# Optimization experiments

Measured on AMD Instinct MI355X. Metric: run time of the kernel, lower is better.

Reference implementation:

```python
import jax, jax.numpy as jnp
import numpy as np

B, S, D, H = 2, 2048, 1024, 16
DH = D // H
SCALE = 1.0 / float(np.sqrt(DH))


def setup_inputs() -> dict:
    key = jax.random.key(0)
    ks = jax.random.split(key, 5)
    x = jax.random.normal(ks[0], (B, S, D), dtype=jnp.float32)
    init = 0.02
    Wq = jax.random.normal(ks[1], (D, D), dtype=jnp.float32) * init
    Wk = jax.random.normal(ks[2], (D, D), dtype=jnp.float32) * init
    Wv = jax.random.normal(ks[3], (D, D), dtype=jnp.float32) * init
    Wo = jax.random.normal(ks[4], (D, D), dtype=jnp.float32) * init
    bq = jnp.zeros((D,), dtype=jnp.float32)
    bk = jnp.zeros((D,), dtype=jnp.float32)
    bv = jnp.zeros((D,), dtype=jnp.float32)
    bo = jnp.zeros((D,), dtype=jnp.float32)
    return {"x": x, "Wq": Wq, "bq": bq, "Wk": Wk, "bk": bk,
            "Wv": Wv, "bv": bv, "Wo": Wo, "bo": bo}


def reference(x, Wq, bq, Wk, bk, Wv, bv, Wo, bo):
    # torch Linear: y = x @ W.T + b  (W: [out, in])
    q = x @ Wq.T + bq  # [B,S,D]
    k = x @ Wk.T + bk
    v = x @ Wv.T + bv
    # split heads -> [B,H,S,dh]
    q = q.reshape(B, S, H, DH).transpose(0, 2, 1, 3)
    k = k.reshape(B, S, H, DH).transpose(0, 2, 1, 3)
    v = v.reshape(B, S, H, DH).transpose(0, 2, 1, 3)
    scores = jnp.einsum('bhqd,bhkd->bhqk', q, k) * SCALE  # [B,H,S,S]
    p = jax.nn.softmax(scores, axis=-1)
    o = jnp.einsum('bhqk,bhkd->bhqd', p, v)  # [B,H,S,dh]
    # faithful to original: view(B, d_model, S) then transpose(-1,-2)
    o = o.reshape(B, D, S).swapaxes(-1, -2)  # [B,S,D]
    return o @ Wo.T + bo
```

## Files before the change

### kernel.cpp

```cpp
#include <hip/hip_runtime.h>
#include <cstdint>
#include <cstddef>


typedef _Float16 h16;
typedef _Float16 h16x8 __attribute__((ext_vector_type(8)));
typedef _Float16 h16x4 __attribute__((ext_vector_type(4)));
typedef float    f32x4 __attribute__((ext_vector_type(4)));

#define MFMA16 __builtin_amdgcn_mfma_f32_16x16x32_f16

#define QSCALE 0.1803368801111204f

__device__ __forceinline__ void gload_lds16(char* lds_dst, const void* gsrc) {
  __builtin_amdgcn_global_load_lds(
      (__attribute__((address_space(1))) void*)gsrc,
      (__attribute__((address_space(3))) void*)lds_dst,
      16, 0, 0);
}


__global__ __launch_bounds__(256)
void cast_all(const float* __restrict__ x,
              const float* __restrict__ wq, const float* __restrict__ wk,
              const float* __restrict__ wv, const float* __restrict__ wo,
              h16* __restrict__ xb, h16* __restrict__ wqb, h16* __restrict__ wkb,
              h16* __restrict__ wvb, h16* __restrict__ wob) {
  const int z = blockIdx.y;
  const float* src; h16* dst; int n4;
  switch (z) {
    case 0:  src = x;  dst = xb;  n4 = 1048576; break;
    case 1:  src = wq; dst = wqb; n4 = 262144;  break;
    case 2:  src = wk; dst = wkb; n4 = 262144;  break;
    case 3:  src = wv; dst = wvb; n4 = 262144;  break;
    default: src = wo; dst = wob; n4 = 262144;  break;
  }
  int i = blockIdx.x * 256 + threadIdx.x;
  const int stride = gridDim.x * 256;
  for (; i < n4; i += stride) {
    float4 v = reinterpret_cast<const float4*>(src)[i];
    h16x4 o = { (h16)v.x, (h16)v.y, (h16)v.z, (h16)v.w };
    reinterpret_cast<h16x4*>(dst)[i] = o;
  }
}

__device__ __forceinline__ void gemm_core_128(
    const h16* __restrict__ A, const h16* __restrict__ W,
    char* lds, f32x4 (&acc)[4][4])
{
  const int tid  = threadIdx.x;
  const int lane = tid & 63;
  const int w    = tid >> 6;
  const int wr   = w >> 1, wc = w & 1;
  const int blockRow = blockIdx.y * 128;
  const int blockCol = blockIdx.x * 128;

  const int sr  = (tid >> 2) & 15;
  const int sc  = tid & 3;
  const int skc = sc ^ ((sr >> 1) & 3);

  const h16* srcA0 = A + (size_t)(blockRow + (0 * 4 + w) * 16 + sr) * 1024 + skc * 8;
  const h16* srcA1 = A + (size_t)(blockRow + (1 * 4 + w) * 16 + sr) * 1024 + skc * 8;
  const h16* srcB0 = W + (size_t)(blockCol + (0 * 4 + w) * 16 + sr) * 1024 + skc * 8;
  const h16* srcB1 = W + (size_t)(blockCol + (1 * 4 + w) * 16 + sr) * 1024 + skc * 8;

  const int dA0o = w * 1024;
  const int dA1o = 4096 + w * 1024;
  const int dB0o = 8192 + w * 1024;
  const int dB1o = 12288 + w * 1024;

  const int fr = lane & 15, fg = lane >> 4;
  const int foff = fr * 64 + ((fg ^ ((fr >> 1) & 3)) << 4);

#pragma unroll
  for (int i = 0; i < 4; ++i)
#pragma unroll
    for (int j = 0; j < 4; ++j) acc[i][j] = f32x4{0.f, 0.f, 0.f, 0.f};

  gload_lds16(lds + dA0o, srcA0);
  gload_lds16(lds + dA1o, srcA1);
  gload_lds16(lds + dB0o, srcB0);
  gload_lds16(lds + dB1o, srcB1);

  for (int ks = 0; ks < 32; ++ks) {
    char* buf = lds + (ks & 1) * 16384;
    __syncthreads();
    if (ks != 31) {
      char* nbuf = lds + ((ks & 1) ^ 1) * 16384;
      gload_lds16(nbuf + dA0o, srcA0 + (ks + 1) * 32);
      gload_lds16(nbuf + dA1o, srcA1 + (ks + 1) * 32);
      gload_lds16(nbuf + dB0o, srcB0 + (ks + 1) * 32);
      gload_lds16(nbuf + dB1o, srcB1 + (ks + 1) * 32);
    }
    char* ldsA = buf;
    char* ldsB = buf + 8192;

    h16x8 af[4], bfv[4];
#pragma unroll
    for (int t = 0; t < 4; ++t)
      af[t] = *(const h16x8*)(ldsA + (wr * 4 + t) * 1024 + foff);
#pragma unroll
    for (int t = 0; t < 4; ++t)
      bfv[t] = *(const h16x8*)(ldsB + (wc * 4 + t) * 1024 + foff);
#pragma unroll
    for (int i = 0; i < 4; ++i)
#pragma unroll
      for (int j = 0; j < 4; ++j)
        acc[i][j] = MFMA16(af[i], bfv[j], acc[i][j], 0, 0, 0);
  }
}

__global__ __launch_bounds__(256, 2)
void gemm_qkv(const h16* __restrict__ xb,
              const h16* __restrict__ wq, const h16* __restrict__ wk, const h16* __restrict__ wv,
              const float* __restrict__ bq, const float* __restrict__ bk, const float* __restrict__ bv,
              h16* __restrict__ q_, h16* __restrict__ k_, h16* __restrict__ vt_)
{
  __shared__ alignas(128) char lds[32768];
  const int z = blockIdx.z;
  const h16* W = (z == 0) ? wq : (z == 1) ? wk : wv;
  const float* bias = (z == 0) ? bq : (z == 1) ? bk : bv;

  f32x4 acc[4][4];
  gemm_core_128(xb, W, lds, acc);

  const int lane = threadIdx.x & 63;
  const int w = threadIdx.x >> 6;
  const int wr = w >> 1, wc = w & 1;
  const int fr = lane & 15, fg = lane >> 4;
  const int blockRow = blockIdx.y * 128;
  const int blockCol = blockIdx.x * 128;

  if (z == 2) {
#pragma unroll
    for (int ct = 0; ct < 4; ++ct) {
      int n = blockCol + wc * 64 + ct * 16 + fr;
      int hh = n >> 6, dd = n & 63;
      float bv_ = bias[n];
#pragma unroll
      for (int rt = 0; rt < 4; ++rt) {
        int m = blockRow + wr * 64 + rt * 16 + 4 * fg;
        int bb = m >> 11, s0 = m & 2047;
        h16x4 pack = { (h16)(acc[rt][ct][0] + bv_), (h16)(acc[rt][ct][1] + bv_),
                       (h16)(acc[rt][ct][2] + bv_), (h16)(acc[rt][ct][3] + bv_) };
        *(h16x4*)(vt_ + ((size_t)((bb * 16 + hh) * 64 + dd)) * 2048 + s0) = pack;
      }
    }
  } else {
    const float scl = (z == 0) ? QSCALE : 1.0f;
    h16* dst = (z == 0) ? q_ : k_;
#pragma unroll
    for (int ct = 0; ct < 4; ++ct) {
      int n = blockCol + wc * 64 + ct * 16 + fr;
      float bv_ = bias[n];
#pragma unroll
      for (int rt = 0; rt < 4; ++rt) {
        int m0 = blockRow + wr * 64 + rt * 16 + 4 * fg;
#pragma unroll
        for (int r = 0; r < 4; ++r)
          dst[(size_t)(m0 + r) * 1024 + n] = (h16)((acc[rt][ct][r] + bv_) * scl);
      }
    }
  }
}

__global__ __launch_bounds__(256, 2)
void gemm_out(const h16* __restrict__ yt, const h16* __restrict__ wo,
              const float* __restrict__ bo, float* __restrict__ out)
{
  __shared__ alignas(128) char lds[32768];
  f32x4 acc[4][4];
  gemm_core_128(yt, wo, lds, acc);

  const int lane = threadIdx.x & 63;
  const int w = threadIdx.x >> 6;
  const int wr = w >> 1, wc = w & 1;
  const int fr = lane & 15, fg = lane >> 4;
  const int blockRow = blockIdx.y * 128;
  const int blockCol = blockIdx.x * 128;

#pragma unroll
  for (int ct = 0; ct < 4; ++ct) {
    int n = blockCol + wc * 64 + ct * 16 + fr;
    float bv_ = bo[n];
#pragma unroll
    for (int rt = 0; rt < 4; ++rt) {
      int m0 = blockRow + wr * 64 + rt * 16 + 4 * fg;
#pragma unroll
      for (int r = 0; r < 4; ++r)
        out[(size_t)(m0 + r) * 1024 + n] = acc[rt][ct][r] + bv_;
    }
  }
}

__global__ __launch_bounds__(256, 2)
void attn_kernel(const h16* __restrict__ qb, const h16* __restrict__ kb,
                 const h16* __restrict__ vtb, h16* __restrict__ ytb)
{
  __shared__ alignas(128) char lds[32768 + 20480];
  const int tid = threadIdx.x, lane = tid & 63, w = tid >> 6;
  const int fr = lane & 15, fg = lane >> 4;

  const int orig = blockIdx.x;
  const int wgid = (orig & 7) * 64 + (orig >> 3);
  const int p  = wgid & 15;
  const int hh = (wgid >> 4) & 15;
  const int b  = wgid >> 8;

  char* ldsP_A = lds + 32768 + w * 5120;
  char* ldsP_B = ldsP_A + 2560;

  const int aq = w * 16 + fr;
  const h16* qrowA = qb + ((size_t)(b * 2048 + 32 * aq + p)) * 1024 + hh * 64;
  const h16* qrowB = qrowA + 16 * 1024;
  h16x8 qfA0 = *(const h16x8*)(qrowA + fg * 8);
  h16x8 qfA1 = *(const h16x8*)(qrowA + 32 + fg * 8);
  h16x8 qfB0 = *(const h16x8*)(qrowB + fg * 8);
  h16x8 qfB1 = *(const h16x8*)(qrowB + 32 + fg * 8);

  const int sr  = (tid >> 2) & 15;
  const int sc  = tid & 3;
  const int skc = sc ^ ((sr >> 1) & 3);
  const int rloc0 = (w >> 1) * 16 + sr;
  const int rloc1 = ((4 + w) >> 1) * 16 + sr;
  const int kc0 = (w & 1) * 32 + skc * 8;
  const int kc1 = ((4 + w) & 1) * 32 + skc * 8;

  const h16* srcK0 = kb + ((size_t)(b * 2048 + rloc0)) * 1024 + hh * 64 + kc0;
  const h16* srcK1 = kb + ((size_t)(b * 2048 + rloc1)) * 1024 + hh * 64 + kc1;
  const h16* srcV0 = vtb + ((size_t)((b * 16 + hh) * 64 + rloc0)) * 2048 + kc0;
  const h16* srcV1 = vtb + ((size_t)((b * 16 + hh) * 64 + rloc1)) * 2048 + kc1;

  const int dK0o = w * 1024, dK1o = 4096 + w * 1024;
  const int dV0o = 8192 + w * 1024, dV1o = 12288 + w * 1024;

  const int foff = fr * 64 + ((fg ^ ((fr >> 1) & 3)) << 4);

  f32x4 oA[4], oB[4];
#pragma unroll
  for (int i = 0; i < 4; ++i) { oA[i] = f32x4{0.f,0.f,0.f,0.f}; oB[i] = f32x4{0.f,0.f,0.f,0.f}; }
  float lA = 0.f, lB = 0.f;

  gload_lds16(lds + dK0o, srcK0);
  gload_lds16(lds + dK1o, srcK1);
  gload_lds16(lds + dV0o, srcV0);
  gload_lds16(lds + dV1o, srcV1);

  for (int ch = 0; ch < 32; ++ch) {
    char* buf = lds + (ch & 1) * 16384;
    __syncthreads();
    if (ch != 31) {
      char* nbuf = lds + ((ch & 1) ^ 1) * 16384;
      gload_lds16(nbuf + dK0o, srcK0 + (size_t)(ch + 1) * 65536);
      gload_lds16(nbuf + dK1o, srcK1 + (size_t)(ch + 1) * 65536);
      gload_lds16(nbuf + dV0o, srcV0 + (size_t)(ch + 1) * 64);
      gload_lds16(nbuf + dV1o, srcV1 + (size_t)(ch + 1) * 64);
    }
    char* ldsK = buf;
    char* ldsV = buf + 8192;

#pragma unroll
    for (int t = 0; t < 4; ++t) {
      h16x8 kf0 = *(const h16x8*)(ldsK + (t * 2 + 0) * 1024 + foff);
      h16x8 kf1 = *(const h16x8*)(ldsK + (t * 2 + 1) * 1024 + foff);
      f32x4 sA = f32x4{0.f,0.f,0.f,0.f};
      sA = MFMA16(kf0, qfA0, sA, 0, 0, 0);
      sA = MFMA16(kf1, qfA1, sA, 0, 0, 0);
      f32x4 sB = f32x4{0.f,0.f,0.f,0.f};
      sB = MFMA16(kf0, qfB0, sB, 0, 0, 0);
      sB = MFMA16(kf1, qfB1, sB, 0, 0, 0);
      float a0 = exp2f(sA[0]), a1 = exp2f(sA[1]), a2 = exp2f(sA[2]), a3 = exp2f(sA[3]);
      float c0 = exp2f(sB[0]), c1 = exp2f(sB[1]), c2 = exp2f(sB[2]), c3 = exp2f(sB[3]);
      h16x4 pkA = { (h16)a0, (h16)a1, (h16)a2, (h16)a3 };
      h16x4 pkB = { (h16)c0, (h16)c1, (h16)c2, (h16)c3 };
      *(h16x4*)(ldsP_A + fr * 160 + t * 32 + fg * 8) = pkA;
      *(h16x4*)(ldsP_B + fr * 160 + t * 32 + fg * 8) = pkB;
      lA += (a0 + a1) + (a2 + a3);
      lB += (c0 + c1) + (c2 + c3);
    }

    h16x8 pfA0 = *(const h16x8*)(ldsP_A + fr * 160 + fg * 16);
    h16x8 pfA1 = *(const h16x8*)(ldsP_A + fr * 160 + 64 + fg * 16);
    h16x8 pfB0 = *(const h16x8*)(ldsP_B + fr * 160 + fg * 16);
    h16x8 pfB1 = *(const h16x8*)(ldsP_B + fr * 160 + 64 + fg * 16);

#pragma unroll
    for (int dt = 0; dt < 4; ++dt) {
      h16x8 vf0 = *(const h16x8*)(ldsV + (dt * 2 + 0) * 1024 + foff);
      h16x8 vf1 = *(const h16x8*)(ldsV + (dt * 2 + 1) * 1024 + foff);
      oA[dt] = MFMA16(pfA0, vf0, oA[dt], 0, 0, 0);
      oA[dt] = MFMA16(pfA1, vf1, oA[dt], 0, 0, 0);
      oB[dt] = MFMA16(pfB0, vf0, oB[dt], 0, 0, 0);
      oB[dt] = MFMA16(pfB1, vf1, oB[dt], 0, 0, 0);
    }
  }

  lA += __shfl_xor(lA, 16); lA += __shfl_xor(lA, 32);
  lB += __shfl_xor(lB, 16); lB += __shfl_xor(lB, 32);
  float iA = 1.0f / lA, iB = 1.0f / lB;
  float iAr[4], iBr[4];
#pragma unroll
  for (int r = 0; r < 4; ++r) {
    int src = (lane & 48) | (4 * fg + r);
    iAr[r] = __shfl(iA, src);
    iBr[r] = __shfl(iB, src);
  }

#pragma unroll
  for (int dt = 0; dt < 4; ++dt) {
    int row = dt * 16 + fr;
    size_t colb = (size_t)(hh * 64 + w * 16 + fg * 4);
    h16x4 sA4 = { (h16)(oA[dt][0] * iAr[0]), (h16)(oA[dt][1] * iAr[1]),
                  (h16)(oA[dt][2] * iAr[2]), (h16)(oA[dt][3] * iAr[3]) };
    h16x4 sB4 = { (h16)(oB[dt][0] * iBr[0]), (h16)(oB[dt][1] * iBr[1]),
                  (h16)(oB[dt][2] * iBr[2]), (h16)(oB[dt][3] * iBr[3]) };
    *(h16x4*)(ytb + ((size_t)(b * 2048 + p * 64 + row)) * 1024 + colb) = sA4;
    *(h16x4*)(ytb + ((size_t)(b * 2048 + (p + 16) * 64 + row)) * 1024 + colb) = sB4;
  }
}

extern "C" void kernel_launch(void* const* d_in, const int* in_sizes, int n_in,
                              void* d_out, int out_size, void* d_ws, size_t ws_size,
                              hipStream_t stream) {
  const float* x  = (const float*)d_in[0];
  const float* Wq = (const float*)d_in[1];
  const float* bq = (const float*)d_in[2];
  const float* Wk = (const float*)d_in[3];
  const float* bk = (const float*)d_in[4];
  const float* Wv = (const float*)d_in[5];
  const float* bv = (const float*)d_in[6];
  const float* Wo = (const float*)d_in[7];
  const float* bo = (const float*)d_in[8];

  char* ws = (char*)d_ws;
  h16* xb  = (h16*)(ws);
  h16* wqb = (h16*)(ws + (size_t)(8  << 20));
  h16* wkb = (h16*)(ws + (size_t)(10 << 20));
  h16* wvb = (h16*)(ws + (size_t)(12 << 20));
  h16* wob = (h16*)(ws + (size_t)(14 << 20));
  h16* q_  = (h16*)(ws + (size_t)(16 << 20));
  h16* k_  = (h16*)(ws + (size_t)(24 << 20));
  h16* vt_ = (h16*)(ws + (size_t)(32 << 20));
  h16* yt_ = (h16*)(ws + (size_t)(40 << 20));

  cast_all<<<dim3(512, 5), 256, 0, stream>>>(x, Wq, Wk, Wv, Wo, xb, wqb, wkb, wvb, wob);
  gemm_qkv<<<dim3(8, 32, 3), 256, 0, stream>>>(xb, wqb, wkb, wvb, bq, bk, bv, q_, k_, vt_);
  attn_kernel<<<512, 256, 0, stream>>>(q_, k_, vt_, yt_);
  gemm_out<<<dim3(8, 32, 1), 256, 0, stream>>>(yt_, wob, bo, (float*)d_out);
}
```

Baseline: 132.0 us.

## Keep softmax probabilities in registers via permlane swaps instead of LDS round-trip

The attention kernel stops writing the exponentiated scores to LDS and reading them back as MFMA A-operands. Instead it packs them with cvt_pkrtz, permutes K rows so the score layout matches the operand layout, and exchanges halves between lanes with v_permlane32_swap. Row sums now use fdot2 on the packed halves, exp2 uses the hardware builtin, and s_setprio brackets the MFMA sections. This removes LDS traffic and one barrier-free dependency per chunk and shrinks LDS use, which may allow more occupancy, at the cost of relying on an exact lane-permutation mapping.

```diff
diff --git a/kernel.cpp b/kernel.cpp
--- a/kernel.cpp
+++ b/kernel.cpp
@@ -6,17 +6,48 @@
 typedef _Float16 h16;
 typedef _Float16 h16x8 __attribute__((ext_vector_type(8)));
 typedef _Float16 h16x4 __attribute__((ext_vector_type(4)));
+typedef _Float16 h16x2 __attribute__((ext_vector_type(2)));
 typedef float    f32x4 __attribute__((ext_vector_type(4)));
+typedef unsigned int u32x4 __attribute__((ext_vector_type(4)));
 
 #define MFMA16 __builtin_amdgcn_mfma_f32_16x16x32_f16
 
 #define QSCALE 0.1803368801111204f
+
+#if __has_builtin(__builtin_amdgcn_exp2f)
+#define EXP2F(x) __builtin_amdgcn_exp2f(x)
+#else
+#define EXP2F(x) exp2f(x)
+#endif
 
 __device__ __forceinline__ void gload_lds16(char* lds_dst, const void* gsrc) {
   __builtin_amdgcn_global_load_lds(
       (__attribute__((address_space(1))) void*)gsrc,
       (__attribute__((address_space(3))) void*)lds_dst,
       16, 0, 0);
+}
+
+__device__ __forceinline__ unsigned pk2(float lo, float hi) {
+  return __builtin_bit_cast(unsigned, __builtin_amdgcn_cvt_pkrtz(lo, hi));
+}
+
+__device__ __forceinline__ float dot2a(unsigned p, float acc) {
+#if __has_builtin(__builtin_amdgcn_fdot2)
+  const h16x2 one = {(h16)1.f, (h16)1.f};
+  return __builtin_amdgcn_fdot2(__builtin_bit_cast(h16x2, p), one, acc, false);
+#else
+  h16x2 v = __builtin_bit_cast(h16x2, p);
+  return acc + (float)v[0] + (float)v[1];
+#endif
+}
+
+__device__ __forceinline__ void swap32(unsigned& a, unsigned& b) {
+  asm("v_permlane32_swap_b32 %0, %1" : "+v"(a), "+v"(b));
+}
+
+__device__ __forceinline__ h16x8 mk8(unsigned u0, unsigned u1, unsigned u2, unsigned u3) {
+  u32x4 v = {u0, u1, u2, u3};
+  return __builtin_bit_cast(h16x8, v);
 }
 
 
@@ -197,7 +228,7 @@
 void attn_kernel(const h16* __restrict__ qb, const h16* __restrict__ kb,
                  const h16* __restrict__ vtb, h16* __restrict__ ytb)
 {
-  __shared__ alignas(128) char lds[32768 + 20480];
+  __shared__ alignas(128) char lds[32768];
   const int tid = threadIdx.x, lane = tid & 63, w = tid >> 6;
   const int fr = lane & 15, fg = lane >> 4;
 
@@ -206,9 +237,6 @@
   const int p  = wgid & 15;
   const int hh = (wgid >> 4) & 15;
   const int b  = wgid >> 8;
-
-  char* ldsP_A = lds + 32768 + w * 5120;
-  char* ldsP_B = ldsP_A + 2560;
 
   const int aq = w * 16 + fr;
   const h16* qrowA = qb + ((size_t)(b * 2048 + 32 * aq + p)) * 1024 + hh * 64;
@@ -235,6 +263,8 @@
   const int dV0o = 8192 + w * 1024, dV1o = 12288 + w * 1024;
 
   const int foff = fr * 64 + ((fg ^ ((fr >> 1) & 3)) << 4);
+  const int sfr  = (fr & 3) | ((fr & 4) << 1) | ((fr & 8) >> 1);
+  const int foffK = sfr * 64 + ((fg ^ ((sfr >> 1) & 3)) << 4);
 
   f32x4 oA[4], oB[4];
 #pragma unroll
@@ -259,31 +289,37 @@
     char* ldsK = buf;
     char* ldsV = buf + 8192;
 
+    unsigned pA[4][2], pB[4][2];
 #pragma unroll
     for (int t = 0; t < 4; ++t) {
-      h16x8 kf0 = *(const h16x8*)(ldsK + (t * 2 + 0) * 1024 + foff);
-      h16x8 kf1 = *(const h16x8*)(ldsK + (t * 2 + 1) * 1024 + foff);
+      h16x8 kf0 = *(const h16x8*)(ldsK + (t * 2 + 0) * 1024 + foffK);
+      h16x8 kf1 = *(const h16x8*)(ldsK + (t * 2 + 1) * 1024 + foffK);
       f32x4 sA = f32x4{0.f,0.f,0.f,0.f};
+      f32x4 sB = f32x4{0.f,0.f,0.f,0.f};
+      __builtin_amdgcn_s_setprio(1);
       sA = MFMA16(kf0, qfA0, sA, 0, 0, 0);
       sA = MFMA16(kf1, qfA1, sA, 0, 0, 0);
-      f32x4 sB = f32x4{0.f,0.f,0.f,0.f};
       sB = MFMA16(kf0, qfB0, sB, 0, 0, 0);
       sB = MFMA16(kf1, qfB1, sB, 0, 0, 0);
-      float a0 = exp2f(sA[0]), a1 = exp2f(sA[1]), a2 = exp2f(sA[2]), a3 = exp2f(sA[3]);
-      float c0 = exp2f(sB[0]), c1 = exp2f(sB[1]), c2 = exp2f(sB[2]), c3 = exp2f(sB[3]);
-      h16x4 pkA = { (h16)a0, (h16)a1, (h16)a2, (h16)a3 };
-      h16x4 pkB = { (h16)c0, (h16)c1, (h16)c2, (h16)c3 };
-      *(h16x4*)(ldsP_A + fr * 160 + t * 32 + fg * 8) = pkA;
-      *(h16x4*)(ldsP_B + fr * 160 + t * 32 + fg * 8) = pkB;
-      lA += (a0 + a1) + (a2 + a3);
-      lB += (c0 + c1) + (c2 + c3);
-    }
-
-    h16x8 pfA0 = *(const h16x8*)(ldsP_A + fr * 160 + fg * 16);
-    h16x8 pfA1 = *(const h16x8*)(ldsP_A + fr * 160 + 64 + fg * 16);
-    h16x8 pfB0 = *(const h16x8*)(ldsP_B + fr * 160 + fg * 16);
-    h16x8 pfB1 = *(const h16x8*)(ldsP_B + fr * 160 + 64 + fg * 16);
-
+      __builtin_amdgcn_s_setprio(0);
+      pA[t][0] = pk2(EXP2F(sA[0]), EXP2F(sA[1]));
+      pA[t][1] = pk2(EXP2F(sA[2]), EXP2F(sA[3]));
+      pB[t][0] = pk2(EXP2F(sB[0]), EXP2F(sB[1]));
+      pB[t][1] = pk2(EXP2F(sB[2]), EXP2F(sB[3]));
+      lA = dot2a(pA[t][0], lA); lA = dot2a(pA[t][1], lA);
+      lB = dot2a(pB[t][0], lB); lB = dot2a(pB[t][1], lB);
+    }
+
+    swap32(pA[0][0], pA[1][0]);  swap32(pA[0][1], pA[1][1]);
+    swap32(pA[2][0], pA[3][0]);  swap32(pA[2][1], pA[3][1]);
+    swap32(pB[0][0], pB[1][0]);  swap32(pB[0][1], pB[1][1]);
+    swap32(pB[2][0], pB[3][0]);  swap32(pB[2][1], pB[3][1]);
+    h16x8 pfA0 = mk8(pA[0][0], pA[0][1], pA[1][0], pA[1][1]);
+    h16x8 pfA1 = mk8(pA[2][0], pA[2][1], pA[3][0], pA[3][1]);
+    h16x8 pfB0 = mk8(pB[0][0], pB[0][1], pB[1][0], pB[1][1]);
+    h16x8 pfB1 = mk8(pB[2][0], pB[2][1], pB[3][0], pB[3][1]);
+
+    __builtin_amdgcn_s_setprio(1);
 #pragma unroll
     for (int dt = 0; dt < 4; ++dt) {
       h16x8 vf0 = *(const h16x8*)(ldsV + (dt * 2 + 0) * 1024 + foff);
@@ -293,6 +329,7 @@
       oB[dt] = MFMA16(pfB0, vf0, oB[dt], 0, 0, 0);
       oB[dt] = MFMA16(pfB1, vf1, oB[dt], 0, 0, 0);
     }
+    __builtin_amdgcn_s_setprio(0);
   }
 
   lA += __shfl_xor(lA, 16); lA += __shfl_xor(lA, 32);
```

Result: faster. 106.8 us (-19.1%).
